# Kernel optimization log

Hardware: AMD Instinct MI355X
Metric: run time of the kernel (lower is better)

Reference implementation:

```python
import jax, jax.numpy as jnp
import numpy as np
import math

# ---- cfg constants (PUMA functional model defaults) ----
XBAR_ROW, XBAR_COL = 128, 128
GON, GOFF, VMAX = 1.0 / 100.0, 1.0 / 600.0, 0.25  # cancel exactly in ideal ADC decode
BIT_SLICE, BIT_STREAM = 2, 1
WEIGHT_BITS, INPUT_BITS = 16, 16
W_FRAC = WEIGHT_BITS // 4 * 3   # 12 fractional bits (default -1 path)
I_FRAC = INPUT_BITS // 4 * 3    # 12
ACM_BITS = 16
ACM_FRAC = ACM_BITS // 4 * 3    # 12 -> accumulator range [-8, 8)
ADC_BIT = int(math.log2(XBAR_ROW)) + BIT_SLICE  # 7 + 2 = 9 (bit_stream==1 adds nothing)
NSLICE = 2 ** BIT_SLICE - 1     # conductance states per slice
NS = WEIGHT_BITS // BIT_SLICE   # 8 weight slices, MSB first
NB = INPUT_BITS // BIT_STREAM   # 16 input bit streams, LSB first


def bit_slicing(w):
    # w: [out, in] nonnegative -> [in, out*NS]; per output col, NS slices MSB first
    wint = jnp.clip(jnp.round(w * 2.0 ** W_FRAC), 0.0, 2.0 ** WEIGHT_BITS - 1)
    shifts = 2.0 ** (BIT_SLICE * jnp.arange(NS - 1, -1, -1, dtype=jnp.float32))
    sl = jnp.floor(wint[:, :, None] / shifts) % (2 ** BIT_SLICE)  # [out,in,NS]
    return sl.transpose(1, 0, 2).reshape(w.shape[1], w.shape[0] * NS)


def to_bits(x):
    # two's-complement fixed-point bits, LSB first -> [B, in, NB]
    xint = jnp.clip(jnp.round(x * 2.0 ** I_FRAC), -(2.0 ** (INPUT_BITS - 1)), 2.0 ** (INPUT_BITS - 1) - 1)
    xint = jnp.where(xint < 0, xint + 2.0 ** INPUT_BITS, xint)
    shifts = 2.0 ** jnp.arange(INPUT_BITS, dtype=jnp.float32)
    return jnp.floor(xint[:, :, None] / shifts) % 2.0


def tile(ws, rt, ct):
    # pad [rows, cols] to crossbar tiles [rt, ct, XBAR_ROW, XBAR_COL]
    pad = jnp.zeros((rt * XBAR_ROW, ct * XBAR_COL), ws.dtype)
    pad = pad.at[:ws.shape[0], :ws.shape[1]].set(ws)
    return pad.reshape(rt, XBAR_ROW, ct, XBAR_COL).transpose(0, 2, 1, 3)


def quant_acm(v):
    lim = 2.0 ** (ACM_BITS - ACM_FRAC - 1)
    q = jnp.round(v * 2.0 ** ACM_FRAC) / 2.0 ** ACM_FRAC
    return jnp.clip(q, -lim, lim - 2.0 ** (-ACM_FRAC))


def crossbar_mvm(bits, slices):
    # bits: [B, R, 128, NB] in {0,1}; slices: [R, C, 128, 128] in {0..NSLICE}
    G = slices * (GON - GOFF) / NSLICE + GOFF          # conductance mapping
    V = bits * VMAX                                     # DAC (1-bit streams)
    # analog column currents per stream: [B, R, C, NB, 128]
    I = jnp.einsum('brks,rckj->brcsj', V, G)
    vsum = V.sum(2)                                     # [B, R, NB]
    # ideal decode: remove Goff offset, rescale to integer dot counts
    counts = (I - vsum[:, :, None, :, None] * GOFF) / (VMAX * (GON - GOFF) / NSLICE)
    # ADC quantization over full-scale range xbar_row*NSLICE with 2**ADC_BIT levels
    step = (XBAR_ROW * NSLICE) / (2.0 ** ADC_BIT - 1)
    counts = jnp.round(counts / step) * step
    B, R, C = counts.shape[:3]
    counts = counts.reshape(B, R, C, NB, XBAR_COL // NS, NS)
    slice_w = 2.0 ** (BIT_SLICE * jnp.arange(NS - 1, -1, -1, dtype=jnp.float32))
    psum = (counts * slice_w).sum(-1)                   # shift-add slices -> [B,R,C,NB,cols]
    stream_w = 2.0 ** jnp.arange(NB, dtype=jnp.float32)
    stream_w = stream_w.at[-1].multiply(-1.0)           # two's-complement MSB is negative
    out = (psum * stream_w[:, None]).sum(3)             # shift-add streams -> [B,R,C,cols]
    out = quant_acm(out / 2.0 ** (W_FRAC + I_FRAC))     # back to float, accumulator quant
    out = out.sum(1)                                    # digital sum over row tiles
    return out.reshape(B, C * (XBAR_COL // NS))


def mvm_forward(x, weight):
    out_f, in_f = weight.shape
    pos = bit_slicing(jnp.clip(weight, 0.0, None))
    neg = bit_slicing(jnp.abs(jnp.clip(weight, None, 0.0)))
    rt = -(-pos.shape[0] // XBAR_ROW)
    ct = -(-pos.shape[1] // XBAR_COL)
    xb_pos, xb_neg = tile(pos, rt, ct), tile(neg, rt, ct)
    bits = to_bits(x)                                   # [B, in, NB]
    B = x.shape[0]
    bits_p = jnp.zeros((B, rt * XBAR_ROW, NB), x.dtype).at[:, :in_f].set(bits)
    bits_p = bits_p.reshape(B, rt, XBAR_ROW, NB)
    out = crossbar_mvm(bits_p, xb_pos) - crossbar_mvm(bits_p, xb_neg)
    return out[:, :out_f]


def setup_inputs() -> dict:
    key = jax.random.key(0)
    k1, k2, k3 = jax.random.split(key, 3)
    x = jax.random.normal(k1, (512, 1024), dtype=jnp.float32) * 0.1
    weight = jax.random.normal(k2, (128, 1024), dtype=jnp.float32) * 0.05
    bias = jax.random.uniform(k3, (128,), dtype=jnp.float32, minval=-0.1, maxval=0.1)
    return {"x": x, "weight": weight, "bias": bias}


def reference(x, weight, bias):
    return mvm_forward(x, weight) + bias[None, :]
```

## Files before the change

kernel.cpp:

```cpp
#include <hip/hip_runtime.h>
#include <stdint.h>

typedef __attribute__((ext_vector_type(4)))  int i32x4;
typedef __attribute__((ext_vector_type(16))) int i32x16;

#define XM_OFF 0u
#define BP_OFF 1048576u

__device__ __forceinline__ uint32_t q16(float v){
  float f = fminf(fmaxf(rintf(v*4096.f), -32768.f), 32767.f);
  return (uint32_t)(int)f & 0xffffu;
}

__global__ __launch_bounds__(256) void pack_k(const float* __restrict__ x, const float* __restrict__ w,
                                              const float* __restrict__ bias,
                                              uint4* __restrict__ xm, uint32_t* __restrict__ Bw,
                                              float* __restrict__ out){
  const int lane = threadIdx.x & 63;
  if (blockIdx.x < 1024){
    int wv = blockIdx.x*4 + (threadIdx.x >> 6);
    int b = wv >> 3, z = wv & 7;
    const float* xp = x + b*1024 + z*128;
    uint32_t u0 = q16(xp[lane]);
    uint32_t u1 = q16(xp[lane + 64]);
    uint4 out4 = {0,0,0,0};
    #pragma unroll
    for (int s = 0; s < 16; ++s){
      unsigned long long m0 = __ballot((u0 >> s) & 1u);
      unsigned long long m1 = __ballot((u1 >> s) & 1u);
      if (lane == s){
        out4.x = (uint32_t)m0; out4.y = (uint32_t)(m0 >> 32);
        out4.z = (uint32_t)m1; out4.w = (uint32_t)(m1 >> 32);
      }
    }
    if (lane < 16) xm[(b*8 + z)*16 + lane] = out4;
  } else if (blockIdx.x < 1152){
    int t = (blockIdx.x - 1024)*256 + threadIdx.x;
    int j = t >> 8, kq = t & 255;
    int r = kq >> 5, kd = kq & 31;
    float4 v = *reinterpret_cast<const float4*>(w + j*1024 + kq*4);
    #pragma unroll
    for (int p = 0; p < 2; ++p){
      uint32_t q0 = (uint32_t)fminf(rintf(fmaxf(p ? -v.x : v.x, 0.f)*4096.f), 65535.f);
      uint32_t q1 = (uint32_t)fminf(rintf(fmaxf(p ? -v.y : v.y, 0.f)*4096.f), 65535.f);
      uint32_t q2 = (uint32_t)fminf(rintf(fmaxf(p ? -v.z : v.z, 0.f)*4096.f), 65535.f);
      uint32_t q3 = (uint32_t)fminf(rintf(fmaxf(p ? -v.w : v.w, 0.f)*4096.f), 65535.f);
      #pragma unroll
      for (int sl = 0; sl < 8; ++sl){
        int sh = 2*(7 - sl);
        uint32_t word = ((q0 >> sh) & 3u) | (((q1 >> sh) & 3u) << 8)
                      | (((q2 >> sh) & 3u) << 16) | (((q3 >> sh) & 3u) << 24);
        Bw[(((r*2 + p)*8 + sl)*128 + j)*32 + kd] = word;
      }
    }
  } else {
    int t = (blockIdx.x - 1152)*256 + threadIdx.x;
    out[t] = rintf(bias[t & 127]*4096.f)*(1.0f/4096.0f);
  }
}

__global__ __launch_bounds__(512, 4) void mvm_main_k(const uint4* __restrict__ xm,
                                                     const uint8_t* __restrict__ Bp,
                                                     float* __restrict__ out){
  __shared__ uint8_t lds[65536];
  __shared__ uint32_t flg[8];
  const int tid = threadIdx.x, lane = tid & 63, wid = tid >> 6;
  const int z = blockIdx.z, jblk = blockIdx.y;
  const int col = lane & 31, hi = lane >> 5;

  {
    const int q = lane >> 3, cS = (lane & 7) ^ q;
    uint32_t f2 = 0;
    #pragma unroll
    for (int u = 0; u < 2; ++u){
      const int si = wid + u*8;
      const uint8_t* src = Bp + ((size_t)((z*16 + si)*128 + jblk*32) << 7);
      uint4 r0 = *(const uint4*)(src + (q     )*128 + cS*16);
      uint4 r1 = *(const uint4*)(src + (q +  8)*128 + cS*16);
      uint4 r2 = *(const uint4*)(src + (q + 16)*128 + cS*16);
      uint4 r3 = *(const uint4*)(src + (q + 24)*128 + cS*16);
      uint8_t* dst = lds + si*4096 + lane*16;
      *(uint4*)(dst       ) = r0;
      *(uint4*)(dst + 1024) = r1;
      *(uint4*)(dst + 2048) = r2;
      *(uint4*)(dst + 3072) = r3;
      uint32_t o = r0.x|r0.y|r0.z|r0.w | r1.x|r1.y|r1.z|r1.w
                 | r2.x|r2.y|r2.z|r2.w | r3.x|r3.y|r3.z|r3.w;
      f2 |= (__any(o != 0u) ? 1u : 0u) << u;
    }
    if (lane == 0) flg[wid] = f2;
  }

  const int bb  = blockIdx.x*32 + wid*4;
  const int s_a = lane & 15;
  const uint4 pwA = xm[((bb     + (col >> 4))*8 + z)*16 + s_a];
  const uint4 pwB = xm[((bb + 2 + (col >> 4))*8 + z)*16 + s_a];
  i32x4 afrA[4], afrB[4];
  {
    const uint32_t wA[4] = {pwA.x, pwA.y, pwA.z, pwA.w};
    const uint32_t wB[4] = {pwB.x, pwB.y, pwB.z, pwB.w};
    #pragma unroll
    for (int f = 0; f < 4; ++f){
      uint32_t plA = wA[f] >> (hi*16);
      uint32_t plB = wB[f] >> (hi*16);
      #pragma unroll
      for (int wI = 0; wI < 4; ++wI){
        afrA[f][wI] = (int)((((plA >> (wI*4)) & 0xFu) * 0x204081u) & 0x01010101u);
        afrB[f][wI] = (int)((((plB >> (wI*4)) & 0xFu) * 0x204081u) & 0x01010101u);
      }
    }
  }
  __syncthreads();

  uint32_t msk = 0;
  #pragma unroll
  for (int w2 = 0; w2 < 8; ++w2){
    uint32_t f2 = flg[w2];
    msk |= (f2 & 1u) << w2;
    msk |= ((f2 >> 1) & 1u) << (w2 + 8);
  }
  msk = (uint32_t)__builtin_amdgcn_readfirstlane((int)msk);

  const int c7 = col & 7;
  const int xo0 = ((0 + hi) ^ c7) << 4;
  const int xo1 = ((2 + hi) ^ c7) << 4;
  const int xo2 = ((4 + hi) ^ c7) << 4;
  const int xo3 = ((6 + hi) ^ c7) << 4;

  i32x16 zz;
  #pragma unroll
  for (int i = 0; i < 16; ++i) zz[i] = 0;

  const float C1 = (float)(511.0/384.0);
  const float QC = (float)(384.0/511.0/4096.0);
  const float sc = hi ? 16.0f : 1.0f;
  const float w7 = hi ? -8.0f : 8.0f;
  float oA0 = 0.f, oA1 = 0.f, oB0 = 0.f, oB1 = 0.f;

  const int pfirst = __builtin_amdgcn_readfirstlane(wid & 1);

#define EPI(cc, A0, A1) do { \
    float nf[16]; \
    _Pragma("unroll") \
    for (int g_ = 0; g_ < 16; ++g_) nf[g_] = rintf((float)cc[g_] * C1); \
    float t0 = fmaf(nf[1], 2.f, nf[0]);  t0 = fmaf(nf[2], 4.f, t0);  t0 = fmaf(nf[3], 8.f, t0); \
    float t1 = fmaf(nf[5], 2.f, nf[4]);  t1 = fmaf(nf[6], 4.f, t1);  t1 = fmaf(nf[7], w7, t1); \
    float t2 = fmaf(nf[9], 2.f, nf[8]);  t2 = fmaf(nf[10],4.f, t2);  t2 = fmaf(nf[11],8.f, t2); \
    float t3 = fmaf(nf[13],2.f, nf[12]); t3 = fmaf(nf[14],4.f, t3);  t3 = fmaf(nf[15],w7, t3); \
    A0 = fmaf(t0, slwv, A0);  A0 = fmaf(t1, slw256, A0); \
    A1 = fmaf(t2, slwv, A1);  A1 = fmaf(t3, slw256, A1); \
  } while (0)

  #pragma unroll
  for (int pi = 0; pi < 2; ++pi){
    const int p = pi ^ pfirst;
    const int tbase = p*8;
    float aA0 = 0.f, aA1 = 0.f, aB0 = 0.f, aB1 = 0.f;
    #pragma unroll
    for (int sl = 0; sl < 8; ++sl){
      if (msk & (1u << (tbase + sl))){
        const float slwv   = (float)(1 << (14 - 2*sl));
        const float slw256 = slwv * 256.0f;
        const uint8_t* lb = lds + (size_t)(tbase + sl)*4096 + col*128;
        i32x4 b0 = *(const i32x4*)(lb + xo0);
        i32x4 b1 = *(const i32x4*)(lb + xo1);
        i32x4 b2 = *(const i32x4*)(lb + xo2);
        i32x4 b3 = *(const i32x4*)(lb + xo3);
        i32x16 cc = __builtin_amdgcn_mfma_i32_32x32x32_i8(afrA[0], b0, zz, 0, 0, 0);
        i32x16 cd = __builtin_amdgcn_mfma_i32_32x32x32_i8(afrB[0], b0, zz, 0, 0, 0);
        cc = __builtin_amdgcn_mfma_i32_32x32x32_i8(afrA[1], b1, cc, 0, 0, 0);
        cd = __builtin_amdgcn_mfma_i32_32x32x32_i8(afrB[1], b1, cd, 0, 0, 0);
        cc = __builtin_amdgcn_mfma_i32_32x32x32_i8(afrA[2], b2, cc, 0, 0, 0);
        cd = __builtin_amdgcn_mfma_i32_32x32x32_i8(afrB[2], b2, cd, 0, 0, 0);
        cc = __builtin_amdgcn_mfma_i32_32x32x32_i8(afrA[3], b3, cc, 0, 0, 0);
        cd = __builtin_amdgcn_mfma_i32_32x32x32_i8(afrB[3], b3, cd, 0, 0, 0);
        EPI(cc, aA0, aA1);
        EPI(cd, aB0, aB1);
      }
    }

    aA0 *= sc; aA1 *= sc; aB0 *= sc; aB1 *= sc;
    aA0 += __shfl_xor(aA0, 32); aA1 += __shfl_xor(aA1, 32);
    aB0 += __shfl_xor(aB0, 32); aB1 += __shfl_xor(aB1, 32);

    float qA0 = fminf(fmaxf(rintf(aA0*QC)*(1.0f/4096.0f), -8.0f), 8.0f - 1.0f/4096.0f);
    float qA1 = fminf(fmaxf(rintf(aA1*QC)*(1.0f/4096.0f), -8.0f), 8.0f - 1.0f/4096.0f);
    float qB0 = fminf(fmaxf(rintf(aB0*QC)*(1.0f/4096.0f), -8.0f), 8.0f - 1.0f/4096.0f);
    float qB1 = fminf(fmaxf(rintf(aB1*QC)*(1.0f/4096.0f), -8.0f), 8.0f - 1.0f/4096.0f);
    const float sgn = p ? -1.0f : 1.0f;
    oA0 = fmaf(qA0, sgn, oA0); oA1 = fmaf(qA1, sgn, oA1);
    oB0 = fmaf(qB0, sgn, oB0); oB1 = fmaf(qB1, sgn, oB1);
  }
#undef EPI

  const int jout = jblk*32 + col;
  atomicAdd(&out[(bb + hi    )*128 + jout], hi ? oA1 : oA0);
  atomicAdd(&out[(bb + 2 + hi)*128 + jout], hi ? oB1 : oB0);
}

extern "C" void kernel_launch(void* const* d_in, const int* in_sizes, int n_in,
                              void* d_out, int out_size, void* d_ws, size_t ws_size,
                              hipStream_t stream){
  const float* x    = (const float*)d_in[0];
  const float* w    = (const float*)d_in[1];
  const float* bias = (const float*)d_in[2];
  uint8_t* ws = (uint8_t*)d_ws;
  float* out = (float*)d_out;

  hipLaunchKernelGGL(pack_k, dim3(1408), dim3(256), 0, stream,
                     x, w, bias, (uint4*)(ws + XM_OFF), (uint32_t*)(ws + BP_OFF), out);
  hipLaunchKernelGGL(mvm_main_k, dim3(16, 4, 8), dim3(512), 0, stream,
                     (const uint4*)(ws + XM_OFF), ws + BP_OFF, out);
}
```

Before: 24.90 us.

## Switch main kernel to 16x16x64 MFMA with smaller column tiles

Replaces the 32x32x32 int8 MFMA tiling (32 batch rows by 32 columns per wave pair) with 16x16x64 MFMA, where each wave handles one batch row's 16 bit-streams against 16 output columns. The grid grows from 512 to 4096 blocks, and the LDS footprint shrinks to 32KB so occupancy can rise (launch bounds 8). The epilogue becomes a 4-element decode plus cross-lane shuffles instead of a 16-element decode. In exchange, the per-block weight tile is reloaded more times across the grid and there are more atomics, one per batch row and column group.

After: 28.80 us. 1.16x slower.

```diff
diff --git a/kernel.cpp b/kernel.cpp
--- a/kernel.cpp
+++ b/kernel.cpp
@@ -2,7 +2,6 @@
 #include <stdint.h>
 
 typedef __attribute__((ext_vector_type(4)))  int i32x4;
-typedef __attribute__((ext_vector_type(16))) int i32x16;
 
 #define XM_OFF 0u
 #define BP_OFF 1048576u
@@ -59,143 +58,98 @@
   }
 }
 
-__global__ __launch_bounds__(512, 4) void mvm_main_k(const uint4* __restrict__ xm,
+__global__ __launch_bounds__(512, 8) void mvm_main_k(const uint4* __restrict__ xm,
                                                      const uint8_t* __restrict__ Bp,
                                                      float* __restrict__ out){
-  __shared__ uint8_t lds[65536];
-  __shared__ uint32_t flg[8];
+  __shared__ uint8_t lds[16*2048];
+  __shared__ uint32_t flg[16];
   const int tid = threadIdx.x, lane = tid & 63, wid = tid >> 6;
-  const int z = blockIdx.z, jblk = blockIdx.y;
-  const int col = lane & 31, hi = lane >> 5;
+  const int bg = blockIdx.x, j16 = blockIdx.y, z = blockIdx.z;
 
   {
-    const int q = lane >> 3, cS = (lane & 7) ^ q;
-    uint32_t f2 = 0;
-    #pragma unroll
-    for (int u = 0; u < 2; ++u){
-      const int si = wid + u*8;
-      const uint8_t* src = Bp + ((size_t)((z*16 + si)*128 + jblk*32) << 7);
-      uint4 r0 = *(const uint4*)(src + (q     )*128 + cS*16);
-      uint4 r1 = *(const uint4*)(src + (q +  8)*128 + cS*16);
-      uint4 r2 = *(const uint4*)(src + (q + 16)*128 + cS*16);
-      uint4 r3 = *(const uint4*)(src + (q + 24)*128 + cS*16);
-      uint8_t* dst = lds + si*4096 + lane*16;
-      *(uint4*)(dst       ) = r0;
-      *(uint4*)(dst + 1024) = r1;
-      *(uint4*)(dst + 2048) = r2;
-      *(uint4*)(dst + 3072) = r3;
-      uint32_t o = r0.x|r0.y|r0.z|r0.w | r1.x|r1.y|r1.z|r1.w
-                 | r2.x|r2.y|r2.z|r2.w | r3.x|r3.y|r3.z|r3.w;
-      f2 |= (__any(o != 0u) ? 1u : 0u) << u;
+    const int si = tid >> 5;
+    const int u  = tid & 31;
+    const int jj = u >> 1, h = u & 1;
+    const uint8_t* src = Bp + (((size_t)((z*16 + si)*128 + j16*16 + jj)) << 7) + h*64;
+    uint4 v0 = *(const uint4*)(src);
+    uint4 v1 = *(const uint4*)(src + 16);
+    uint4 v2 = *(const uint4*)(src + 32);
+    uint4 v3 = *(const uint4*)(src + 48);
+    uint8_t* drow = lds + si*2048 + jj*128;
+    const int m = jj & 7;
+    *(uint4*)(drow + (size_t)(((h*4 + 0) ^ m) << 4)) = v0;
+    *(uint4*)(drow + (size_t)(((h*4 + 1) ^ m) << 4)) = v1;
+    *(uint4*)(drow + (size_t)(((h*4 + 2) ^ m) << 4)) = v2;
+    *(uint4*)(drow + (size_t)(((h*4 + 3) ^ m) << 4)) = v3;
+    uint32_t nz = v0.x|v0.y|v0.z|v0.w | v1.x|v1.y|v1.z|v1.w
+                | v2.x|v2.y|v2.z|v2.w | v3.x|v3.y|v3.z|v3.w;
+    unsigned long long bal = __ballot(nz != 0u);
+    if (lane == 0){
+      flg[wid*2]     = ((uint32_t)bal)         ? 1u : 0u;
+      flg[wid*2 + 1] = ((uint32_t)(bal >> 32)) ? 1u : 0u;
     }
-    if (lane == 0) flg[wid] = f2;
   }
 
-  const int bb  = blockIdx.x*32 + wid*4;
-  const int s_a = lane & 15;
-  const uint4 pwA = xm[((bb     + (col >> 4))*8 + z)*16 + s_a];
-  const uint4 pwB = xm[((bb + 2 + (col >> 4))*8 + z)*16 + s_a];
-  i32x4 afrA[4], afrB[4];
-  {
-    const uint32_t wA[4] = {pwA.x, pwA.y, pwA.z, pwA.w};
-    const uint32_t wB[4] = {pwB.x, pwB.y, pwB.z, pwB.w};
-    #pragma unroll
-    for (int f = 0; f < 4; ++f){
-      uint32_t plA = wA[f] >> (hi*16);
-      uint32_t plB = wB[f] >> (hi*16);
-      #pragma unroll
-      for (int wI = 0; wI < 4; ++wI){
-        afrA[f][wI] = (int)((((plA >> (wI*4)) & 0xFu) * 0x204081u) & 0x01010101u);
-        afrB[f][wI] = (int)((((plB >> (wI*4)) & 0xFu) * 0x204081u) & 0x01010101u);
-      }
-    }
+  const int b = bg*8 + wid;
+  const int s = lane & 15, g = lane >> 4;
+  const uint4 pw = xm[(b*8 + z)*16 + s];
+  uint32_t bits_a = (((g & 2) ? pw.y : pw.x) >> ((g & 1)*16)) & 0xFFFFu;
+  uint32_t bits_b = (((g & 2) ? pw.w : pw.z) >> ((g & 1)*16)) & 0xFFFFu;
+  i32x4 A0, A1;
+  #pragma unroll
+  for (int r = 0; r < 4; ++r){
+    A0[r] = (int)((((bits_a >> (r*4)) & 0xFu) * 0x204081u) & 0x01010101u);
+    A1[r] = (int)((((bits_b >> (r*4)) & 0xFu) * 0x204081u) & 0x01010101u);
   }
   __syncthreads();
 
   uint32_t msk = 0;
   #pragma unroll
-  for (int w2 = 0; w2 < 8; ++w2){
-    uint32_t f2 = flg[w2];
-    msk |= (f2 & 1u) << w2;
-    msk |= ((f2 >> 1) & 1u) << (w2 + 8);
-  }
+  for (int i = 0; i < 16; ++i) msk |= (flg[i] ? 1u : 0u) << i;
   msk = (uint32_t)__builtin_amdgcn_readfirstlane((int)msk);
 
-  const int c7 = col & 7;
-  const int xo0 = ((0 + hi) ^ c7) << 4;
-  const int xo1 = ((2 + hi) ^ c7) << 4;
-  const int xo2 = ((4 + hi) ^ c7) << 4;
-  const int xo3 = ((6 + hi) ^ c7) << 4;
+  const int jm = s & 7;
+  const int o0 = s*128 + ((g    ) ^ jm)*16;
+  const int o1 = s*128 + ((g + 4) ^ jm)*16;
 
-  i32x16 zz;
-  #pragma unroll
-  for (int i = 0; i < 16; ++i) zz[i] = 0;
-
+  const i32x4 zz4 = {0, 0, 0, 0};
   const float C1 = (float)(511.0/384.0);
   const float QC = (float)(384.0/511.0/4096.0);
-  const float sc = hi ? 16.0f : 1.0f;
-  const float w7 = hi ? -8.0f : 8.0f;
-  float oA0 = 0.f, oA1 = 0.f, oB0 = 0.f, oB1 = 0.f;
+  const float w3 = (g == 3) ? -8.0f : 8.0f;
+  const float vf = (float)(1 << (4*g));
 
-  const int pfirst = __builtin_amdgcn_readfirstlane(wid & 1);
-
-#define EPI(cc, A0, A1) do { \
-    float nf[16]; \
-    _Pragma("unroll") \
-    for (int g_ = 0; g_ < 16; ++g_) nf[g_] = rintf((float)cc[g_] * C1); \
-    float t0 = fmaf(nf[1], 2.f, nf[0]);  t0 = fmaf(nf[2], 4.f, t0);  t0 = fmaf(nf[3], 8.f, t0); \
-    float t1 = fmaf(nf[5], 2.f, nf[4]);  t1 = fmaf(nf[6], 4.f, t1);  t1 = fmaf(nf[7], w7, t1); \
-    float t2 = fmaf(nf[9], 2.f, nf[8]);  t2 = fmaf(nf[10],4.f, t2);  t2 = fmaf(nf[11],8.f, t2); \
-    float t3 = fmaf(nf[13],2.f, nf[12]); t3 = fmaf(nf[14],4.f, t3);  t3 = fmaf(nf[15],w7, t3); \
-    A0 = fmaf(t0, slwv, A0);  A0 = fmaf(t1, slw256, A0); \
-    A1 = fmaf(t2, slwv, A1);  A1 = fmaf(t3, slw256, A1); \
-  } while (0)
-
+  float acc[2] = {0.f, 0.f};
   #pragma unroll
-  for (int pi = 0; pi < 2; ++pi){
-    const int p = pi ^ pfirst;
-    const int tbase = p*8;
-    float aA0 = 0.f, aA1 = 0.f, aB0 = 0.f, aB1 = 0.f;
+  for (int p = 0; p < 2; ++p){
     #pragma unroll
     for (int sl = 0; sl < 8; ++sl){
-      if (msk & (1u << (tbase + sl))){
-        const float slwv   = (float)(1 << (14 - 2*sl));
-        const float slw256 = slwv * 256.0f;
-        const uint8_t* lb = lds + (size_t)(tbase + sl)*4096 + col*128;
-        i32x4 b0 = *(const i32x4*)(lb + xo0);
-        i32x4 b1 = *(const i32x4*)(lb + xo1);
-        i32x4 b2 = *(const i32x4*)(lb + xo2);
-        i32x4 b3 = *(const i32x4*)(lb + xo3);
-        i32x16 cc = __builtin_amdgcn_mfma_i32_32x32x32_i8(afrA[0], b0, zz, 0, 0, 0);
-        i32x16 cd = __builtin_amdgcn_mfma_i32_32x32x32_i8(afrB[0], b0, zz, 0, 0, 0);
-        cc = __builtin_amdgcn_mfma_i32_32x32x32_i8(afrA[1], b1, cc, 0, 0, 0);
-        cd = __builtin_amdgcn_mfma_i32_32x32x32_i8(afrB[1], b1, cd, 0, 0, 0);
-        cc = __builtin_amdgcn_mfma_i32_32x32x32_i8(afrA[2], b2, cc, 0, 0, 0);
-        cd = __builtin_amdgcn_mfma_i32_32x32x32_i8(afrB[2], b2, cd, 0, 0, 0);
-        cc = __builtin_amdgcn_mfma_i32_32x32x32_i8(afrA[3], b3, cc, 0, 0, 0);
-        cd = __builtin_amdgcn_mfma_i32_32x32x32_i8(afrB[3], b3, cd, 0, 0, 0);
-        EPI(cc, aA0, aA1);
-        EPI(cd, aB0, aB1);
+      const int ti = p*8 + sl;
+      if (msk & (1u << ti)){
+        const uint8_t* lb = lds + ti*2048;
+        i32x4 B0 = *(const i32x4*)(lb + o0);
+        i32x4 B1 = *(const i32x4*)(lb + o1);
+        i32x4 cc = __builtin_amdgcn_mfma_i32_16x16x64_i8(A0, B0, zz4, 0, 0, 0);
+        cc = __builtin_amdgcn_mfma_i32_16x16x64_i8(A1, B1, cc, 0, 0, 0);
+        float nf0 = rintf((float)cc[0] * C1);
+        float nf1 = rintf((float)cc[1] * C1);
+        float nf2 = rintf((float)cc[2] * C1);
+        float nf3 = rintf((float)cc[3] * C1);
+        float t = fmaf(nf1, 2.f, nf0);
+        t = fmaf(nf2, 4.f, t);
+        t = fmaf(nf3, w3, t);
+        const float slwvf = (float)(1 << (14 - 2*sl)) * vf;
+        acc[p] = fmaf(t, slwvf, acc[p]);
       }
     }
+  }
 
-    aA0 *= sc; aA1 *= sc; aB0 *= sc; aB1 *= sc;
-    aA0 += __shfl_xor(aA0, 32); aA1 += __shfl_xor(aA1, 32);
-    aB0 += __shfl_xor(aB0, 32); aB1 += __shfl_xor(aB1, 32);
-
-    float qA0 = fminf(fmaxf(rintf(aA0*QC)*(1.0f/4096.0f), -8.0f), 8.0f - 1.0f/4096.0f);
-    float qA1 = fminf(fmaxf(rintf(aA1*QC)*(1.0f/4096.0f), -8.0f), 8.0f - 1.0f/4096.0f);
-    float qB0 = fminf(fmaxf(rintf(aB0*QC)*(1.0f/4096.0f), -8.0f), 8.0f - 1.0f/4096.0f);
-    float qB1 = fminf(fmaxf(rintf(aB1*QC)*(1.0f/4096.0f), -8.0f), 8.0f - 1.0f/4096.0f);
-    const float sgn = p ? -1.0f : 1.0f;
-    oA0 = fmaf(qA0, sgn, oA0); oA1 = fmaf(qA1, sgn, oA1);
-    oB0 = fmaf(qB0, sgn, oB0); oB1 = fmaf(qB1, sgn, oB1);
-  }
-#undef EPI
-
-  const int jout = jblk*32 + col;
-  atomicAdd(&out[(bb + hi    )*128 + jout], hi ? oA1 : oA0);
-  atomicAdd(&out[(bb + 2 + hi)*128 + jout], hi ? oB1 : oB0);
+  float a0 = acc[0];
+  a0 += __shfl_xor(a0, 16); a0 += __shfl_xor(a0, 32);
+  float a1 = acc[1];
+  a1 += __shfl_xor(a1, 16); a1 += __shfl_xor(a1, 32);
+  float q0 = fminf(fmaxf(rintf(a0*QC)*(1.0f/4096.0f), -8.0f), 8.0f - 1.0f/4096.0f);
+  float q1 = fminf(fmaxf(rintf(a1*QC)*(1.0f/4096.0f), -8.0f), 8.0f - 1.0f/4096.0f);
+  if (lane < 16) atomicAdd(&out[b*128 + j16*16 + lane], q0 - q1);
 }
 
 extern "C" void kernel_launch(void* const* d_in, const int* in_sizes, int n_in,
@@ -209,6 +163,6 @@
 
   hipLaunchKernelGGL(pack_k, dim3(1408), dim3(256), 0, stream,
                      x, w, bias, (uint4*)(ws + XM_OFF), (uint32_t*)(ws + BP_OFF), out);
-  hipLaunchKernelGGL(mvm_main_k, dim3(16, 4, 8), dim3(512), 0, stream,
+  hipLaunchKernelGGL(mvm_main_k, dim3(64, 8, 8), dim3(512), 0, stream,
                      (const uint4*)(ws + XM_OFF), ws + BP_OFF, out);
 }
```

## Precompute nonzero slice masks in pack, compact LDS staging, halve batch per block

Applied to the files above, without the earlier changes.

The pack kernel now computes a per-row-tile, per-column-block bitmask of which weight slices are nonzero and stores it in workspace. The main kernel reads the mask up front and loads only the nonzero slices into a compacted LDS buffer of 13 slots, falling back to global loads for any extra slices. It also halves the batch rows per block and doubles the grid, with one MFMA chain per wave and launch bounds raised to 6. The intent is to cut wasted slice loads and LDS use so occupancy rises. The cost is more atomics and less A-operand reuse per B load.

After: 25.36 us. About the same (+1.8%).

```diff
diff --git a/kernel.cpp b/kernel.cpp
--- a/kernel.cpp
+++ b/kernel.cpp
@@ -6,6 +6,7 @@
 
 #define XM_OFF 0u
 #define BP_OFF 1048576u
+#define MK_OFF 3145728u
 
 __device__ __forceinline__ uint32_t q16(float v){
   float f = fminf(fmaxf(rintf(v*4096.f), -32768.f), 32767.f);
@@ -15,7 +16,7 @@
 __global__ __launch_bounds__(256) void pack_k(const float* __restrict__ x, const float* __restrict__ w,
                                               const float* __restrict__ bias,
                                               uint4* __restrict__ xm, uint32_t* __restrict__ Bw,
-                                              float* __restrict__ out){
+                                              uint16_t* __restrict__ mk, float* __restrict__ out){
   const int lane = threadIdx.x & 63;
   if (blockIdx.x < 1024){
     int wv = blockIdx.x*4 + (threadIdx.x >> 6);
@@ -39,6 +40,7 @@
     int j = t >> 8, kq = t & 255;
     int r = kq >> 5, kd = kq & 31;
     float4 v = *reinterpret_cast<const float4*>(w + j*1024 + kq*4);
+    uint32_t lm = 0;
     #pragma unroll
     for (int p = 0; p < 2; ++p){
       uint32_t q0 = (uint32_t)fminf(rintf(fmaxf(p ? -v.x : v.x, 0.f)*4096.f), 65535.f);
@@ -51,75 +53,75 @@
         uint32_t word = ((q0 >> sh) & 3u) | (((q1 >> sh) & 3u) << 8)
                       | (((q2 >> sh) & 3u) << 16) | (((q3 >> sh) & 3u) << 24);
         Bw[(((r*2 + p)*8 + sl)*128 + j)*32 + kd] = word;
-      }
-    }
+        lm |= (word != 0u ? 1u : 0u) << (p*8 + sl);
+      }
+    }
+    lm |= (uint32_t)__shfl_xor((int)lm, 16);
+    lm |= (uint32_t)__shfl_xor((int)lm, 8);
+    lm |= (uint32_t)__shfl_xor((int)lm, 4);
+    lm |= (uint32_t)__shfl_xor((int)lm, 2);
+    lm |= (uint32_t)__shfl_xor((int)lm, 1);
+    if ((threadIdx.x & 31) == 0) mk[r*128 + j] = (uint16_t)lm;
   } else {
     int t = (blockIdx.x - 1152)*256 + threadIdx.x;
     out[t] = rintf(bias[t & 127]*4096.f)*(1.0f/4096.0f);
   }
 }
 
-__global__ __launch_bounds__(512, 4) void mvm_main_k(const uint4* __restrict__ xm,
+__global__ __launch_bounds__(512, 6) void mvm_main_k(const uint4* __restrict__ xm,
                                                      const uint8_t* __restrict__ Bp,
+                                                     const uint16_t* __restrict__ mk,
                                                      float* __restrict__ out){
-  __shared__ uint8_t lds[65536];
-  __shared__ uint32_t flg[8];
+  __shared__ uint8_t lds[13*4096];
   const int tid = threadIdx.x, lane = tid & 63, wid = tid >> 6;
   const int z = blockIdx.z, jblk = blockIdx.y;
   const int col = lane & 31, hi = lane >> 5;
 
+  uint32_t mv = ((const uint32_t*)mk)[z*64 + jblk*16 + (lane & 15)];
+  mv |= (uint32_t)__shfl_xor((int)mv, 1);
+  mv |= (uint32_t)__shfl_xor((int)mv, 2);
+  mv |= (uint32_t)__shfl_xor((int)mv, 4);
+  mv |= (uint32_t)__shfl_xor((int)mv, 8);
+  const uint32_t msk = (uint32_t)__builtin_amdgcn_readfirstlane((int)((mv | (mv >> 16)) & 0xFFFFu));
+
   {
     const int q = lane >> 3, cS = (lane & 7) ^ q;
-    uint32_t f2 = 0;
-    #pragma unroll
-    for (int u = 0; u < 2; ++u){
-      const int si = wid + u*8;
-      const uint8_t* src = Bp + ((size_t)((z*16 + si)*128 + jblk*32) << 7);
-      uint4 r0 = *(const uint4*)(src + (q     )*128 + cS*16);
-      uint4 r1 = *(const uint4*)(src + (q +  8)*128 + cS*16);
-      uint4 r2 = *(const uint4*)(src + (q + 16)*128 + cS*16);
-      uint4 r3 = *(const uint4*)(src + (q + 24)*128 + cS*16);
-      uint8_t* dst = lds + si*4096 + lane*16;
-      *(uint4*)(dst       ) = r0;
-      *(uint4*)(dst + 1024) = r1;
-      *(uint4*)(dst + 2048) = r2;
-      *(uint4*)(dst + 3072) = r3;
-      uint32_t o = r0.x|r0.y|r0.z|r0.w | r1.x|r1.y|r1.z|r1.w
-                 | r2.x|r2.y|r2.z|r2.w | r3.x|r3.y|r3.z|r3.w;
-      f2 |= (__any(o != 0u) ? 1u : 0u) << u;
-    }
-    if (lane == 0) flg[wid] = f2;
-  }
-
-  const int bb  = blockIdx.x*32 + wid*4;
+    int slot = 0;
+    #pragma unroll
+    for (int ti = 0; ti < 16; ++ti){
+      if (msk & (1u << ti)){
+        if ((slot == wid || slot == wid + 8) && slot < 13){
+          const uint8_t* src = Bp + ((size_t)((z*16 + ti)*128 + jblk*32) << 7);
+          uint4 r0 = *(const uint4*)(src + (q     )*128 + cS*16);
+          uint4 r1 = *(const uint4*)(src + (q +  8)*128 + cS*16);
+          uint4 r2 = *(const uint4*)(src + (q + 16)*128 + cS*16);
+          uint4 r3 = *(const uint4*)(src + (q + 24)*128 + cS*16);
+          uint8_t* dst = lds + slot*4096 + lane*16;
+          *(uint4*)(dst       ) = r0;
+          *(uint4*)(dst + 1024) = r1;
+          *(uint4*)(dst + 2048) = r2;
+          *(uint4*)(dst + 3072) = r3;
+        }
+        ++slot;
+      }
+    }
+  }
+
+  const int bb  = blockIdx.x*16 + wid*2;
   const int s_a = lane & 15;
-  const uint4 pwA = xm[((bb     + (col >> 4))*8 + z)*16 + s_a];
-  const uint4 pwB = xm[((bb + 2 + (col >> 4))*8 + z)*16 + s_a];
-  i32x4 afrA[4], afrB[4];
+  const uint4 pw = xm[((bb + (col >> 4))*8 + z)*16 + s_a];
+  i32x4 afr[4];
   {
-    const uint32_t wA[4] = {pwA.x, pwA.y, pwA.z, pwA.w};
-    const uint32_t wB[4] = {pwB.x, pwB.y, pwB.z, pwB.w};
+    const uint32_t wd[4] = {pw.x, pw.y, pw.z, pw.w};
     #pragma unroll
     for (int f = 0; f < 4; ++f){
-      uint32_t plA = wA[f] >> (hi*16);
-      uint32_t plB = wB[f] >> (hi*16);
+      uint32_t pl = wd[f] >> (hi*16);
       #pragma unroll
-      for (int wI = 0; wI < 4; ++wI){
-        afrA[f][wI] = (int)((((plA >> (wI*4)) & 0xFu) * 0x204081u) & 0x01010101u);
-        afrB[f][wI] = (int)((((plB >> (wI*4)) & 0xFu) * 0x204081u) & 0x01010101u);
-      }
+      for (int wI = 0; wI < 4; ++wI)
+        afr[f][wI] = (int)((((pl >> (wI*4)) & 0xFu) * 0x204081u) & 0x01010101u);
     }
   }
   __syncthreads();
-
-  uint32_t msk = 0;
-  #pragma unroll
-  for (int w2 = 0; w2 < 8; ++w2){
-    uint32_t f2 = flg[w2];
-    msk |= (f2 & 1u) << w2;
-    msk |= ((f2 >> 1) & 1u) << (w2 + 8);
-  }
-  msk = (uint32_t)__builtin_amdgcn_readfirstlane((int)msk);
 
   const int c7 = col & 7;
   const int xo0 = ((0 + hi) ^ c7) << 4;
@@ -135,9 +137,7 @@
   const float QC = (float)(384.0/511.0/4096.0);
   const float sc = hi ? 16.0f : 1.0f;
   const float w7 = hi ? -8.0f : 8.0f;
-  float oA0 = 0.f, oA1 = 0.f, oB0 = 0.f, oB1 = 0.f;
-
-  const int pfirst = __builtin_amdgcn_readfirstlane(wid & 1);
+  float a00 = 0.f, a01 = 0.f, a10 = 0.f, a11 = 0.f;
 
 #define EPI(cc, A0, A1) do { \
     float nf[16]; \
@@ -151,51 +151,51 @@
     A1 = fmaf(t2, slwv, A1);  A1 = fmaf(t3, slw256, A1); \
   } while (0)
 
-  #pragma unroll
-  for (int pi = 0; pi < 2; ++pi){
-    const int p = pi ^ pfirst;
-    const int tbase = p*8;
-    float aA0 = 0.f, aA1 = 0.f, aB0 = 0.f, aB1 = 0.f;
-    #pragma unroll
-    for (int sl = 0; sl < 8; ++sl){
-      if (msk & (1u << (tbase + sl))){
+  {
+    int slot2 = 0;
+    #pragma unroll
+    for (int ti = 0; ti < 16; ++ti){
+      if (msk & (1u << ti)){
+        const int sl = ti & 7;
         const float slwv   = (float)(1 << (14 - 2*sl));
         const float slw256 = slwv * 256.0f;
-        const uint8_t* lb = lds + (size_t)(tbase + sl)*4096 + col*128;
-        i32x4 b0 = *(const i32x4*)(lb + xo0);
-        i32x4 b1 = *(const i32x4*)(lb + xo1);
-        i32x4 b2 = *(const i32x4*)(lb + xo2);
-        i32x4 b3 = *(const i32x4*)(lb + xo3);
-        i32x16 cc = __builtin_amdgcn_mfma_i32_32x32x32_i8(afrA[0], b0, zz, 0, 0, 0);
-        i32x16 cd = __builtin_amdgcn_mfma_i32_32x32x32_i8(afrB[0], b0, zz, 0, 0, 0);
-        cc = __builtin_amdgcn_mfma_i32_32x32x32_i8(afrA[1], b1, cc, 0, 0, 0);
-        cd = __builtin_amdgcn_mfma_i32_32x32x32_i8(afrB[1], b1, cd, 0, 0, 0);
-        cc = __builtin_amdgcn_mfma_i32_32x32x32_i8(afrA[2], b2, cc, 0, 0, 0);
-        cd = __builtin_amdgcn_mfma_i32_32x32x32_i8(afrB[2], b2, cd, 0, 0, 0);
-        cc = __builtin_amdgcn_mfma_i32_32x32x32_i8(afrA[3], b3, cc, 0, 0, 0);
-        cd = __builtin_amdgcn_mfma_i32_32x32x32_i8(afrB[3], b3, cd, 0, 0, 0);
-        EPI(cc, aA0, aA1);
-        EPI(cd, aB0, aB1);
-      }
-    }
-
-    aA0 *= sc; aA1 *= sc; aB0 *= sc; aB1 *= sc;
-    aA0 += __shfl_xor(aA0, 32); aA1 += __shfl_xor(aA1, 32);
-    aB0 += __shfl_xor(aB0, 32); aB1 += __shfl_xor(aB1, 32);
-
-    float qA0 = fminf(fmaxf(rintf(aA0*QC)*(1.0f/4096.0f), -8.0f), 8.0f - 1.0f/4096.0f);
-    float qA1 = fminf(fmaxf(rintf(aA1*QC)*(1.0f/4096.0f), -8.0f), 8.0f - 1.0f/4096.0f);
-    float qB0 = fminf(fmaxf(rintf(aB0*QC)*(1.0f/4096.0f), -8.0f), 8.0f - 1.0f/4096.0f);
-    float qB1 = fminf(fmaxf(rintf(aB1*QC)*(1.0f/4096.0f), -8.0f), 8.0f - 1.0f/4096.0f);
-    const float sgn = p ? -1.0f : 1.0f;
-    oA0 = fmaf(qA0, sgn, oA0); oA1 = fmaf(qA1, sgn, oA1);
-    oB0 = fmaf(qB0, sgn, oB0); oB1 = fmaf(qB1, sgn, oB1);
+        i32x4 b0, b1, b2, b3;
+        if (slot2 < 13){
+          const uint8_t* lb = lds + slot2*4096 + col*128;
+          b0 = *(const i32x4*)(lb + xo0);
+          b1 = *(const i32x4*)(lb + xo1);
+          b2 = *(const i32x4*)(lb + xo2);
+          b3 = *(const i32x4*)(lb + xo3);
+        } else {
+          const uint8_t* gb = Bp + ((size_t)((z*16 + ti)*128 + jblk*32 + col) << 7) + hi*16;
+          b0 = *(const i32x4*)(gb      );
+          b1 = *(const i32x4*)(gb + 32 );
+          b2 = *(const i32x4*)(gb + 64 );
+          b3 = *(const i32x4*)(gb + 96 );
+        }
+        i32x16 cc = __builtin_amdgcn_mfma_i32_32x32x32_i8(afr[0], b0, zz, 0, 0, 0);
+        cc = __builtin_amdgcn_mfma_i32_32x32x32_i8(afr[1], b1, cc, 0, 0, 0);
+        cc = __builtin_amdgcn_mfma_i32_32x32x32_i8(afr[2], b2, cc, 0, 0, 0);
+        cc = __builtin_amdgcn_mfma_i32_32x32x32_i8(afr[3], b3, cc, 0, 0, 0);
+        if (ti < 8) EPI(cc, a00, a01);
+        else        EPI(cc, a10, a11);
+        ++slot2;
+      }
+    }
   }
 #undef EPI
 
+  a00 *= sc; a01 *= sc; a10 *= sc; a11 *= sc;
+  a00 += __shfl_xor(a00, 32); a01 += __shfl_xor(a01, 32);
+  a10 += __shfl_xor(a10, 32); a11 += __shfl_xor(a11, 32);
+  float q00 = fminf(fmaxf(rintf(a00*QC)*(1.0f/4096.0f), -8.0f), 8.0f - 1.0f/4096.0f);
+  float q01 = fminf(fmaxf(rintf(a01*QC)*(1.0f/4096.0f), -8.0f), 8.0f - 1.0f/4096.0f);
+  float q10 = fminf(fmaxf(rintf(a10*QC)*(1.0f/4096.0f), -8.0f), 8.0f - 1.0f/4096.0f);
+  float q11 = fminf(fmaxf(rintf(a11*QC)*(1.0f/4096.0f), -8.0f), 8.0f - 1.0f/4096.0f);
+  const float o0 = q00 - q10;
+  const float o1 = q01 - q11;
   const int jout = jblk*32 + col;
-  atomicAdd(&out[(bb + hi    )*128 + jout], hi ? oA1 : oA0);
-  atomicAdd(&out[(bb + 2 + hi)*128 + jout], hi ? oB1 : oB0);
+  atomicAdd(&out[(bb + hi)*128 + jout], hi ? o1 : o0);
 }
 
 extern "C" void kernel_launch(void* const* d_in, const int* in_sizes, int n_in,
@@ -208,7 +208,9 @@
   float* out = (float*)d_out;
 
   hipLaunchKernelGGL(pack_k, dim3(1408), dim3(256), 0, stream,
-                     x, w, bias, (uint4*)(ws + XM_OFF), (uint32_t*)(ws + BP_OFF), out);
-  hipLaunchKernelGGL(mvm_main_k, dim3(16, 4, 8), dim3(512), 0, stream,
-                     (const uint4*)(ws + XM_OFF), ws + BP_OFF, out);
-}
+                     x, w, bias, (uint4*)(ws + XM_OFF), (uint32_t*)(ws + BP_OFF),
+                     (uint16_t*)(ws + MK_OFF), out);
+  hipLaunchKernelGGL(mvm_main_k, dim3(32, 4, 8), dim3(512), 0, stream,
+                     (const uint4*)(ws + XM_OFF), ws + BP_OFF,
+                     (const uint16_t*)(ws + MK_OFF), out);
+}
```
